# Performance work log

Hardware: AMD Instinct MI355X
Metric: run time of the kernel (lower is better)

## Reference

```python
import jax, jax.numpy as jnp
import numpy as np

B, SQ, SK, D = 16, 2048, 2048, 64


def setup_inputs() -> dict:
    key = jax.random.key(0)
    k1, k2, k3, k4 = jax.random.split(key, 4)
    return {
        "query": jax.random.normal(k1, (B, SQ, D), dtype=jnp.float32),
        "key": jax.random.normal(k2, (B, SK, D), dtype=jnp.float32),
        "value": jax.random.normal(k3, (B, SK, D), dtype=jnp.float32),
        "mask": jax.random.randint(k4, (B, SQ, SK), 0, 2).astype(bool),
    }


def reference(query, key, value, mask):
    # score = Q K^T / sqrt(D); masked positions -> -inf
    scale = 1.0 / jnp.sqrt(jnp.asarray(query.shape[-1], query.dtype))
    score = jnp.einsum("bqd,bkd->bqk", query, key) * scale  # [B, SQ, SK]
    score = jnp.where(mask, -jnp.inf, score)
    attn = jax.nn.softmax(score, axis=-1)
    context = jnp.einsum("bqk,bkd->bqd", attn, value)  # [B, SQ, D]
    return (context, attn)
```

## Files before the change

kernel.cpp:

```cpp
#include <hip/hip_runtime.h>
#include <hip/hip_bf16.h>

typedef __attribute__((ext_vector_type(8))) __bf16   bf16x8;
typedef __attribute__((ext_vector_type(4))) _Float16 f16x4;
typedef __attribute__((ext_vector_type(8))) _Float16 f16x8;
typedef __attribute__((ext_vector_type(4))) float    f32x4;
typedef __attribute__((ext_vector_type(4))) int      i32x4;
typedef __attribute__((ext_vector_type(8))) unsigned short u16x8;

namespace {
constexpr int kB   = 16;
constexpr int kSQ  = 2048;
constexpr int kSK  = 2048;
constexpr int kD   = 64;
constexpr int kQB  = 16;
constexpr int kNW  = 4;
constexpr int kTPW = 32;
constexpr int kNT  = kSK / 16;
constexpr int kCStride = 68;
constexpr int kStgStride = 144;
constexpr float kScaleLog2e = 0.18033688011112042f;
constexpr size_t kVpOff   = 4u << 20;
constexpr size_t kBitsOff = 8u << 20;
}

__global__ __launch_bounds__(256)
void conv_k(const float* __restrict__ K, unsigned short* __restrict__ Kp)
{
  const int idx = blockIdx.x * 256 + threadIdx.x;
  const int lam = idx & 63, f = (idx >> 6) & 1, kt = (idx >> 7) & (kNT - 1),
            b = idx >> 14;
  const int l15 = lam & 15, kg = lam >> 4;
  const float* src = K + ((size_t)(b * kSK + kt * 16 + l15) * kD) + f * 32 + kg * 8;
  u16x8 o;
#pragma unroll
  for (int e = 0; e < 8; ++e) {
    union { float f; unsigned int u; } cv; cv.f = src[e];
    unsigned int r = cv.u + 0x7fff + ((cv.u >> 16) & 1);
    o[e] = (unsigned short)(r >> 16);
  }
  *reinterpret_cast<u16x8*>(Kp + (size_t)idx * 8) = o;
}

__global__ __launch_bounds__(256)
void conv_v(const float* __restrict__ V, _Float16* __restrict__ Vp)
{
  const int idx = blockIdx.x * 256 + threadIdx.x;
  const int h = idx & 1, lam = (idx >> 1) & 63, t = (idx >> 7) & (kNT - 1),
            b = idx >> 14;
  const int l15 = lam & 15, kg = lam >> 4;
  f16x8 o;
#pragma unroll
  for (int j = 0; j < 2; ++j)
#pragma unroll
    for (int e = 0; e < 4; ++e)
      o[j * 4 + e] = (_Float16)
          V[((size_t)(b * kSK + t * 16 + kg * 4 + e) * kD) + (2 * h + j) * 16 + l15];
  *reinterpret_cast<f16x8*>(Vp + (size_t)idx * 8) = o;
}

__global__ __launch_bounds__(256)
void conv_m(const int* __restrict__ M, unsigned long long* __restrict__ bits)
{
  const int gtid = blockIdx.x * 256 + threadIdx.x;
  const int wv   = gtid >> 6;
  const int lane = gtid & 63;
  const size_t ibase = (size_t)wv * 4096;
  unsigned long long myword = 0;
#pragma unroll
  for (int j = 0; j < 64; ++j) {
    const int v = M[ibase + (size_t)j * 64 + lane];
    const unsigned long long bb = __ballot(v != 0);
    myword = (lane == j) ? bb : myword;
  }
  bits[(size_t)wv * 64 + lane] = myword;
}

__global__ __launch_bounds__(256, 3)
void sdpa_main(const float* __restrict__ Qg, const unsigned short* __restrict__ Kp,
               const _Float16* __restrict__ Vp, const unsigned int* __restrict__ Mbits,
               float* __restrict__ ctxOut, float* __restrict__ attnOut)
{
  __shared__ float sums[kNW][kQB];
  __shared__ __align__(16) float cpart[kNW][kQB][kCStride];
  __shared__ __align__(16) char stg[kNW * kQB * kStgStride];

  const int tid  = threadIdx.x;
  const int wid  = tid >> 6;
  const int lane = tid & 63;
  const int l15  = lane & 15;
  const int kg   = lane >> 4;

  const int wg = (blockIdx.x & 7) * 256 + (blockIdx.x >> 3);
  const int b  = wg >> 7;
  const int q0 = (wg & 127) * kQB;

  const float* Qb = Qg + (size_t)b * kSQ * kD;
  const int qrow  = q0 + l15;
  const int kbase = wid * (kTPW * 16);
  const int gt0   = wid * kTPW;

  const unsigned short* Kpb = Kp + (size_t)b * kNT * 2 * 64 * 8;
  const _Float16*       Vpb = Vp + (size_t)b * kNT * 64 * 16;

  bf16x8 qf0, qf1;
  {
    const float* qp = Qb + (size_t)qrow * kD + kg * 8;
#pragma unroll
    for (int e = 0; e < 8; ++e) { qf0[e] = (__bf16)qp[e]; qf1[e] = (__bf16)qp[32 + e]; }
  }

  unsigned int mw[16];
  {
    const unsigned int* mwp = Mbits + ((size_t)(b * kSQ + qrow) * (kSK / 32))
                                     + (kbase >> 5);
#pragma unroll
    for (int i = 0; i < 4; ++i) {
      const i32x4 v = *reinterpret_cast<const i32x4*>(mwp + i * 4);
#pragma unroll
      for (int j = 0; j < 4; ++j) mw[i * 4 + j] = (unsigned int)v[j];
    }
  }

  auto kfrag = [&](int t, int f) {
    return *reinterpret_cast<const bf16x8*>(
        Kpb + (((size_t)(gt0 + t) * 2 + f) * 64 + lane) * 8);
  };

  f16x4 pb[kTPW];
  float lsum = 0.f;
  bf16x8 kb0[2], kb1[2];
  kb0[0] = kfrag(0, 0); kb1[0] = kfrag(0, 1);
#pragma unroll
  for (int t = 0; t < kTPW; ++t) {
    const int cur = t & 1, nxt = cur ^ 1;
    if (t + 1 < kTPW) { kb0[nxt] = kfrag(t + 1, 0); kb1[nxt] = kfrag(t + 1, 1); }
    f32x4 acc = {0.f, 0.f, 0.f, 0.f};
    acc = __builtin_amdgcn_mfma_f32_16x16x32_bf16(kb0[cur], qf0, acc, 0, 0, 0);
    acc = __builtin_amdgcn_mfma_f32_16x16x32_bf16(kb1[cur], qf1, acc, 0, 0, 0);
    const unsigned int bits4 =
        (mw[t >> 1] >> (((t & 1) << 4) + (kg << 2))) & 15u;
    f16x4 p4;
#pragma unroll
    for (int r = 0; r < 4; ++r) {
      const float pv = ((bits4 >> r) & 1u)
                           ? 0.f
                           : __builtin_amdgcn_exp2f(acc[r] * kScaleLog2e);
      lsum += pv;
      p4[r] = (_Float16)pv;
    }
    pb[t] = p4;
  }
  lsum += __shfl_xor(lsum, 16, 64);
  lsum += __shfl_xor(lsum, 32, 64);
  if (lane < 16) sums[wid][l15] = lsum;
  __syncthreads();

  {
    const int r0 = lane >> 3, r1 = r0 + 8;
    float la = 0.f, lb = 0.f;
#pragma unroll
    for (int w = 0; w < kNW; ++w) { la += sums[w][r0]; lb += sums[w][r1]; }
    const float invA = 1.0f / la, invB = 1.0f / lb;
    char* sw = stg + wid * (kQB * kStgStride);
    const int c8 = (lane & 7) * 8;
    float* arow0 = attnOut + ((size_t)b * kSQ + q0 + r0) * kSK + kbase;
    float* arow1 = attnOut + ((size_t)b * kSQ + q0 + r1) * kSK + kbase;
#pragma unroll
    for (int g = 0; g < 8; ++g) {
#pragma unroll
      for (int tl = 0; tl < 4; ++tl)
        *reinterpret_cast<f16x4*>(sw + l15 * kStgStride + tl * 32 + kg * 8)
            = pb[g * 4 + tl];
      const f16x4 x0a = *reinterpret_cast<const f16x4*>(sw + r0 * kStgStride + c8);
      const f16x4 x0b = *reinterpret_cast<const f16x4*>(sw + r0 * kStgStride + 64 + c8);
      const f16x4 x1a = *reinterpret_cast<const f16x4*>(sw + r1 * kStgStride + c8);
      const f16x4 x1b = *reinterpret_cast<const f16x4*>(sw + r1 * kStgStride + 64 + c8);
      float4 o;
      const int cA = g * 64 + (lane & 7) * 4;
      o.x = (float)x0a[0] * invA; o.y = (float)x0a[1] * invA;
      o.z = (float)x0a[2] * invA; o.w = (float)x0a[3] * invA;
      *reinterpret_cast<float4*>(arow0 + cA) = o;
      o.x = (float)x0b[0] * invA; o.y = (float)x0b[1] * invA;
      o.z = (float)x0b[2] * invA; o.w = (float)x0b[3] * invA;
      *reinterpret_cast<float4*>(arow0 + cA + 32) = o;
      o.x = (float)x1a[0] * invB; o.y = (float)x1a[1] * invB;
      o.z = (float)x1a[2] * invB; o.w = (float)x1a[3] * invB;
      *reinterpret_cast<float4*>(arow1 + cA) = o;
      o.x = (float)x1b[0] * invB; o.y = (float)x1b[1] * invB;
      o.z = (float)x1b[2] * invB; o.w = (float)x1b[3] * invB;
      *reinterpret_cast<float4*>(arow1 + cA + 32) = o;
    }
  }

  f32x4 cacc[4];
#pragma unroll
  for (int d = 0; d < 4; ++d) cacc[d] = f32x4{0.f, 0.f, 0.f, 0.f};
  f16x8 v01[2], v23[2];
  {
    const _Float16* vb = Vpb + ((size_t)gt0 * 64 + lane) * 16;
    v01[0] = *reinterpret_cast<const f16x8*>(vb);
    v23[0] = *reinterpret_cast<const f16x8*>(vb + 8);
  }
#pragma unroll
  for (int t = 0; t < kTPW; ++t) {
    const int cur = t & 1, nxt = cur ^ 1;
    if (t + 1 < kTPW) {
      const _Float16* vb = Vpb + ((size_t)(gt0 + t + 1) * 64 + lane) * 16;
      v01[nxt] = *reinterpret_cast<const f16x8*>(vb);
      v23[nxt] = *reinterpret_cast<const f16x8*>(vb + 8);
    }
    const f16x4 pfrag = pb[t];
    union { f16x8 v; f16x4 h[2]; } a, c;
    a.v = v01[cur]; c.v = v23[cur];
    cacc[0] = __builtin_amdgcn_mfma_f32_16x16x16f16(a.h[0], pfrag, cacc[0], 0, 0, 0);
    cacc[1] = __builtin_amdgcn_mfma_f32_16x16x16f16(a.h[1], pfrag, cacc[1], 0, 0, 0);
    cacc[2] = __builtin_amdgcn_mfma_f32_16x16x16f16(c.h[0], pfrag, cacc[2], 0, 0, 0);
    cacc[3] = __builtin_amdgcn_mfma_f32_16x16x16f16(c.h[1], pfrag, cacc[3], 0, 0, 0);
  }
#pragma unroll
  for (int dblk = 0; dblk < 4; ++dblk)
    *reinterpret_cast<f32x4*>(&cpart[wid][l15][dblk * 16 + kg * 4]) = cacc[dblk];
  __syncthreads();

  {
    const int q = tid >> 4;
    const int d = (tid & 15) * 4;
    float4 o = make_float4(0.f, 0.f, 0.f, 0.f);
#pragma unroll
    for (int w = 0; w < kNW; ++w) {
      const float4 p = *reinterpret_cast<const float4*>(&cpart[w][q][d]);
      o.x += p.x; o.y += p.y; o.z += p.z; o.w += p.w;
    }
    float l = 0.f;
#pragma unroll
    for (int w = 0; w < kNW; ++w) l += sums[w][q];
    const float iv = 1.0f / l;
    o.x *= iv; o.y *= iv; o.z *= iv; o.w *= iv;
    *reinterpret_cast<float4*>(ctxOut + ((size_t)b * kSQ + q0 + q) * kD + d) = o;
  }
}

extern "C" void kernel_launch(void* const* d_in, const int* in_sizes, int n_in,
                              void* d_out, int out_size, void* d_ws, size_t ws_size,
                              hipStream_t stream)
{
  const float* Q = (const float*)d_in[0];
  const float* K = (const float*)d_in[1];
  const float* V = (const float*)d_in[2];
  const int*   M = (const int*)d_in[3];
  float* ctx  = (float*)d_out;
  float* attn = (float*)d_out + (size_t)kB * kSQ * kD;

  unsigned short*     Kp = (unsigned short*)d_ws;
  _Float16*           Vp = (_Float16*)((char*)d_ws + kVpOff);
  unsigned long long* Mb = (unsigned long long*)((char*)d_ws + kBitsOff);

  hipLaunchKernelGGL(conv_k, dim3(1024), dim3(256), 0, stream, K, Kp);
  hipLaunchKernelGGL(conv_v, dim3(1024), dim3(256), 0, stream, V, Vp);
  hipLaunchKernelGGL(conv_m, dim3(4096), dim3(256), 0, stream, M, Mb);
  hipLaunchKernelGGL(sdpa_main, dim3(kB * kSQ / kQB), dim3(256), 0, stream,
                     Q, Kp, Vp, (const unsigned int*)Mb, ctx, attn);
}
```

Before: 185.4 us.

## Fuse mask bit-packing into attention kernel via LDS ballot

Drops the separate conv_m pass that packed the int mask into a bitmask in global workspace. Each workgroup now reads its own 16 mask rows directly, packs them with wave ballots into shared memory, and builds per-lane mask words from there. This saves one kernel launch and the write and re-read of the bitmask. In exchange the mask-read latency now sits in the main kernel's prologue behind a barrier. The occupancy hint is also raised from 3 to 4 blocks per CU, which may pressure registers.

```diff
diff --git a/kernel.cpp b/kernel.cpp
--- a/kernel.cpp
+++ b/kernel.cpp
@@ -20,8 +20,7 @@
 constexpr int kCStride = 68;
 constexpr int kStgStride = 144;
 constexpr float kScaleLog2e = 0.18033688011112042f;
-constexpr size_t kVpOff   = 4u << 20;
-constexpr size_t kBitsOff = 8u << 20;
+constexpr size_t kVpOff = 4u << 20;
 }
 
 __global__ __launch_bounds__(256)
@@ -59,31 +58,15 @@
   *reinterpret_cast<f16x8*>(Vp + (size_t)idx * 8) = o;
 }
 
-__global__ __launch_bounds__(256)
-void conv_m(const int* __restrict__ M, unsigned long long* __restrict__ bits)
-{
-  const int gtid = blockIdx.x * 256 + threadIdx.x;
-  const int wv   = gtid >> 6;
-  const int lane = gtid & 63;
-  const size_t ibase = (size_t)wv * 4096;
-  unsigned long long myword = 0;
-#pragma unroll
-  for (int j = 0; j < 64; ++j) {
-    const int v = M[ibase + (size_t)j * 64 + lane];
-    const unsigned long long bb = __ballot(v != 0);
-    myword = (lane == j) ? bb : myword;
-  }
-  bits[(size_t)wv * 64 + lane] = myword;
-}
-
-__global__ __launch_bounds__(256, 3)
+__global__ __launch_bounds__(256, 4)
 void sdpa_main(const float* __restrict__ Qg, const unsigned short* __restrict__ Kp,
-               const _Float16* __restrict__ Vp, const unsigned int* __restrict__ Mbits,
+               const _Float16* __restrict__ Vp, const int* __restrict__ Mg,
                float* __restrict__ ctxOut, float* __restrict__ attnOut)
 {
   __shared__ float sums[kNW][kQB];
   __shared__ __align__(16) float cpart[kNW][kQB][kCStride];
   __shared__ __align__(16) char stg[kNW * kQB * kStgStride];
+  __shared__ __align__(16) unsigned long long bitsLds[kQB][34];
 
   const int tid  = threadIdx.x;
   const int wid  = tid >> 6;
@@ -110,13 +93,30 @@
     for (int e = 0; e < 8; ++e) { qf0[e] = (__bf16)qp[e]; qf1[e] = (__bf16)qp[32 + e]; }
   }
 
+  {
+    const int* mbase = Mg + (size_t)b * kSQ * kSK;
+#pragma unroll
+    for (int p = 0; p < 2; ++p) {
+      unsigned long long myword = 0;
+#pragma unroll
+      for (int i = 0; i < 64; ++i) {
+        const int rl = wid * 4 + p * 2 + (i >> 5);
+        const int v  = mbase[(size_t)(q0 + rl) * kSK + (i & 31) * 64 + lane];
+        const unsigned long long bb = __ballot(v != 0);
+        if (lane == i) myword = bb;
+      }
+      bitsLds[wid * 4 + p * 2 + (lane >> 5)][lane & 31] = myword;
+    }
+  }
+  __syncthreads();
+
   unsigned int mw[16];
   {
-    const unsigned int* mwp = Mbits + ((size_t)(b * kSQ + qrow) * (kSK / 32))
-                                     + (kbase >> 5);
+    const unsigned int* rowbits =
+        reinterpret_cast<const unsigned int*>(&bitsLds[l15][0]) + wid * 16;
 #pragma unroll
     for (int i = 0; i < 4; ++i) {
-      const i32x4 v = *reinterpret_cast<const i32x4*>(mwp + i * 4);
+      const i32x4 v = *reinterpret_cast<const i32x4*>(rowbits + i * 4);
 #pragma unroll
       for (int j = 0; j < 4; ++j) mw[i * 4 + j] = (unsigned int)v[j];
     }
@@ -252,13 +252,11 @@
   float* ctx  = (float*)d_out;
   float* attn = (float*)d_out + (size_t)kB * kSQ * kD;
 
-  unsigned short*     Kp = (unsigned short*)d_ws;
-  _Float16*           Vp = (_Float16*)((char*)d_ws + kVpOff);
-  unsigned long long* Mb = (unsigned long long*)((char*)d_ws + kBitsOff);
+  unsigned short* Kp = (unsigned short*)d_ws;
+  _Float16*       Vp = (_Float16*)((char*)d_ws + kVpOff);
 
   hipLaunchKernelGGL(conv_k, dim3(1024), dim3(256), 0, stream, K, Kp);
   hipLaunchKernelGGL(conv_v, dim3(1024), dim3(256), 0, stream, V, Vp);
-  hipLaunchKernelGGL(conv_m, dim3(4096), dim3(256), 0, stream, M, Mb);
   hipLaunchKernelGGL(sdpa_main, dim3(kB * kSQ / kQB), dim3(256), 0, stream,
-                     Q, Kp, Vp, (const unsigned int*)Mb, ctx, attn);
-}
+                     Q, Kp, Vp, M, ctx, attn);
+}
```

After: 259.3 us. +39.9%, slower.
